# Kernel optimization log

Hardware: AMD Instinct MI355X
Metric: run time of the kernel (lower is better)

## Reference

```python
import jax, jax.numpy as jnp
import numpy as np

NUM_HEADS = 2
DIM_NODE = 100
DIM_EDGE = 100
DIM_TIME = 100
DIM_OUT = 100
N_DST = 32768
N_EDGE = 524288
LN_EPS = 1e-5


def setup_inputs() -> dict:
    key = jax.random.key(0)
    ks = jax.random.split(key, 12)
    dst_h = jax.random.normal(ks[0], (N_DST, DIM_NODE), dtype=jnp.float32)
    src_h = jax.random.normal(ks[1], (N_EDGE, DIM_NODE), dtype=jnp.float32)
    efeat = jax.random.normal(ks[2], (N_EDGE, DIM_EDGE), dtype=jnp.float32)
    # time deltas are non-negative elapsed times
    time_deltas = jax.random.uniform(ks[3], (N_EDGE,), dtype=jnp.float32) * 1000.0
    edge_dst = jnp.sort(jax.random.randint(ks[4], (N_EDGE,), 0, N_DST, dtype=jnp.int32))
    # TimeEncode: fixed geometric frequencies, zero bias
    time_w = jnp.asarray(1.0 / 10 ** np.linspace(0, 9, DIM_TIME), dtype=jnp.float32)
    time_b = jnp.zeros((DIM_TIME,), dtype=jnp.float32)
    def lin(k, fan_out, fan_in):
        s = 1.0 / np.sqrt(fan_in)
        return jax.random.uniform(k, (fan_out, fan_in), jnp.float32, -s, s)
    wq_w = lin(ks[5], DIM_OUT, DIM_NODE + DIM_TIME)
    wq_b = jax.random.normal(ks[6], (DIM_OUT,), jnp.float32) * 0.02
    wkv_w = lin(ks[7], 2 * DIM_OUT, DIM_NODE + DIM_EDGE + DIM_TIME)
    wkv_b = jax.random.normal(ks[8], (2 * DIM_OUT,), jnp.float32) * 0.02
    wout_w = lin(ks[9], DIM_OUT, DIM_NODE + DIM_OUT)
    wout_b = jax.random.normal(ks[10], (DIM_OUT,), jnp.float32) * 0.02
    ln_g = jnp.ones((DIM_OUT,), jnp.float32)
    ln_b = jnp.zeros((DIM_OUT,), jnp.float32)
    return dict(dst_h=dst_h, src_h=src_h, efeat=efeat, time_deltas=time_deltas,
                edge_dst=edge_dst, time_w=time_w, time_b=time_b,
                wq_w=wq_w, wq_b=wq_b, wkv_w=wkv_w, wkv_b=wkv_b,
                wout_w=wout_w, wout_b=wout_b, ln_g=ln_g, ln_b=ln_b)


def reference(dst_h, src_h, efeat, time_deltas, edge_dst, time_w, time_b,
              wq_w, wq_b, wkv_w, wkv_b, wout_w, wout_b, ln_g, ln_b):
    n_dst = dst_h.shape[0]
    dim_out = wq_w.shape[0]
    dh = dim_out // NUM_HEADS
    # TimeEncode: cos(w*t + b); zero-time feature for dst nodes
    zero_tf = jnp.broadcast_to(jnp.cos(time_b), (n_dst, time_b.shape[0]))
    nbr_tf = jnp.cos(time_deltas[:, None] * time_w[None, :] + time_b)  # [E, dim_time]
    Q = jnp.concatenate([dst_h, zero_tf], axis=1) @ wq_w.T + wq_b       # [N_dst, dim_out]
    Z = jnp.concatenate([src_h, efeat, nbr_tf], axis=1) @ wkv_w.T + wkv_b  # [E, 2*dim_out]
    K = Z[:, :dim_out].reshape(-1, NUM_HEADS, dh)
    V = Z[:, dim_out:].reshape(-1, NUM_HEADS, dh)
    Qe = Q[edge_dst].reshape(-1, NUM_HEADS, dh)  # edge_view gather
    attn = jnp.sum(Qe * K, axis=2)               # [E, H]
    attn = jax.nn.leaky_relu(attn, negative_slope=0.2)
    # edge_softmax: segment softmax over edges grouped by dst
    m = jax.ops.segment_max(attn, edge_dst, num_segments=n_dst)
    e = jnp.exp(attn - m[edge_dst])
    s = jax.ops.segment_sum(e, edge_dst, num_segments=n_dst)
    a = e / s[edge_dst]                           # [E, H]
    out_e = (V * a[:, :, None]).reshape(-1, dim_out)
    out = jax.ops.segment_sum(out_e, edge_dst, num_segments=n_dst)  # edge_reduce sum
    out = jnp.concatenate([out, dst_h], axis=1) @ wout_w.T + wout_b
    out = jax.nn.relu(out)  # dropout disabled (eval)
    mu = jnp.mean(out, axis=-1, keepdims=True)
    var = jnp.var(out, axis=-1, keepdims=True)
    return (out - mu) / jnp.sqrt(var + LN_EPS) * ln_g + ln_b
```

## Files before the change

### kernel.cpp

```cpp
#include <hip/hip_runtime.h>
#include <math.h>

#define N_DST   32768
#define N_EDGE  524288
#define LN_EPS  1e-5f

typedef __attribute__((ext_vector_type(8))) short short8b;
typedef __attribute__((ext_vector_type(4))) float f32x4;

static __device__ __forceinline__ unsigned short f2bf(float f) {
    unsigned u = __float_as_uint(f);
    u += 0x7fff + ((u >> 16) & 1);
    return (unsigned short)(u >> 16);
}
static __device__ __forceinline__ float bf2f(unsigned short s) {
    return __uint_as_float(((unsigned)s) << 16);
}

__global__ void k_prep(const float* __restrict__ wkv_w, const float* __restrict__ wq_w,
                       const float* __restrict__ wq_b, const float* __restrict__ time_b,
                       const float* __restrict__ wout_w,
                       float* __restrict__ zq, float* __restrict__ wout_t,
                       unsigned short* __restrict__ Bv) {
    int idx = blockIdx.x * 256 + threadIdx.x;
    if (idx < 100) {
        float acc = wq_b[idx];
        for (int j = 0; j < 100; ++j)
            acc += cosf(time_b[j]) * wq_w[idx * 200 + 100 + j];
        zq[idx] = acc;
    } else if (idx < 20100) {
        int r = idx - 100;
        wout_t[r] = wout_w[(size_t)(r % 100) * 200 + r / 100];
    } else if (idx < 95364) {
        int r2 = idx - 20100;
        int jj = r2 & 7, l = (r2 >> 3) & 63, nf = (r2 >> 9) % 7, kc = r2 / 3584;
        int j = kc * 32 + ((l >> 4) << 3) + jj;
        int o = nf * 16 + (l & 15);
        float v = (j < 600 && o < 100 && (j / 300 == o / 50))
                  ? wkv_w[(size_t)(100 + o) * 300 + (j % 300)] : 0.f;
        Bv[r2] = f2bf(v);
    }
}

__global__ void k_precomp(const float* __restrict__ wq_w, const float* __restrict__ wkv_w,
                          const float* __restrict__ wkv_b, const float* __restrict__ zq,
                          unsigned short* __restrict__ Bq, float* __restrict__ C2) {
    int idx = blockIdx.x * 256 + threadIdx.x;
    if (idx < 77824) {
        int jj = idx & 7, l = (idx >> 3) & 63, nf = (idx >> 9) % 19, kcp = idx / 9728;
        int kc = kcp & 3, p = kcp >> 2;
        int i = kc * 32 + ((l >> 4) << 3) + jj;
        int j = p * 304 + nf * 16 + (l & 15);
        float acc = 0.f;
        if (i < 100 && j < 602) {
            if (j < 600) {
                int h = j / 300, cc = j % 300;
                const float* __restrict__ wq = wq_w + (size_t)(h * 50) * 200 + i;
                const float* __restrict__ wk = wkv_w + (size_t)(h * 50) * 300 + cc;
                #pragma unroll 10
                for (int d = 0; d < 50; ++d)
                    acc = fmaf(wq[(size_t)d * 200], wk[(size_t)d * 300], acc);
            } else {
                int h = j - 600;
                const float* __restrict__ wq = wq_w + (size_t)(h * 50) * 200 + i;
                for (int d = 0; d < 50; ++d)
                    acc = fmaf(wq[(size_t)d * 200], wkv_b[h * 50 + d], acc);
            }
        }
        Bq[idx] = f2bf(acc);
    } else if (idx < 78426) {
        int j = idx - 77824;
        float acc = 0.f;
        if (j < 600) {
            int h = j / 300, cc = j % 300;
            for (int d = 0; d < 50; ++d)
                acc = fmaf(zq[h * 50 + d], wkv_w[(size_t)(h * 50 + d) * 300 + cc], acc);
        } else {
            int h = j - 600;
            for (int d = 0; d < 50; ++d)
                acc = fmaf(zq[h * 50 + d], wkv_b[h * 50 + d], acc);
        }
        C2[j] = acc;
    }
}

__global__ void k_offsets(const int* __restrict__ dst, int* __restrict__ off) {
    int n = blockIdx.x * 256 + threadIdx.x;
    if (n > N_DST) return;
    int lo = 0, hi = N_EDGE;
    while (lo < hi) {
        int mid = (lo + hi) >> 1;
        if (dst[mid] < n) lo = mid + 1; else hi = mid;
    }
    off[n] = lo;
}

__global__ __launch_bounds__(256, 1) void k_qw(
        const float* __restrict__ dst_h, const unsigned short* __restrict__ Bq,
        const float* __restrict__ C2, unsigned short* __restrict__ QW) {
    __shared__ alignas(16) unsigned short Bs[9728];
    const int t = threadIdx.x, lane = t & 63;
    const int g = blockIdx.x * 4 + (t >> 6);
    const int col = lane & 15, slice = lane >> 4;
    const int row = g * 16 + col;

    short8b af[4];
    {
        const float* __restrict__ dr = dst_h + (size_t)row * 100;
        #pragma unroll
        for (int kc = 0; kc < 4; ++kc) {
            int k0 = kc * 32 + slice * 8;
            float4 xa = make_float4(0.f, 0.f, 0.f, 0.f), xb = xa;
            if (k0 + 8 <= 100) { xa = *(const float4*)(dr + k0); xb = *(const float4*)(dr + k0 + 4); }
            else if (k0 < 100)  { xa = *(const float4*)(dr + k0); }
            short8b a;
            a[0] = (short)f2bf(xa.x); a[1] = (short)f2bf(xa.y);
            a[2] = (short)f2bf(xa.z); a[3] = (short)f2bf(xa.w);
            a[4] = (short)f2bf(xb.x); a[5] = (short)f2bf(xb.y);
            a[6] = (short)f2bf(xb.z); a[7] = (short)f2bf(xb.w);
            af[kc] = a;
        }
    }
    const int re0 = g * 16 + (slice << 2);
    #pragma unroll
    for (int p = 0; p < 2; ++p) {
        f32x4 acc[19];
        #pragma unroll
        for (int nf = 0; nf < 19; ++nf) {
            int c = p * 304 + nf * 16 + col;
            float b = (c < 602) ? C2[c] : 0.f;
            acc[nf] = (f32x4){b, b, b, b};
        }
        #pragma unroll
        for (int kc = 0; kc < 4; ++kc) {
            {
                const float4* __restrict__ ws4 = (const float4*)Bq + (size_t)(p * 4 + kc) * 1216;
                float4* __restrict__ wd = (float4*)Bs;
                #pragma unroll
                for (int i = 0; i < 4; ++i) wd[i * 256 + t] = ws4[i * 256 + t];
                if (t < 192) wd[1024 + t] = ws4[1024 + t];
            }
            __syncthreads();
            #pragma unroll
            for (int nf = 0; nf < 19; ++nf) {
                short8b w = *(const short8b*)(&Bs[(size_t)(nf * 64 + lane) * 8]);
                acc[nf] = __builtin_amdgcn_mfma_f32_16x16x32_bf16(af[kc], w, acc[nf], 0, 0, 0);
            }
            __syncthreads();
        }
        #pragma unroll
        for (int nf = 0; nf < 19; ++nf) {
            int c = p * 304 + nf * 16 + col;
            if (c < 602) {
                #pragma unroll
                for (int r = 0; r < 4; ++r)
                    QW[(size_t)(re0 + r) * 608 + c] = f2bf(acc[nf][r]);
            }
        }
    }
}

__global__ __launch_bounds__(256) void k_node(
        const float* __restrict__ src_h, const float* __restrict__ efeat,
        const float* __restrict__ td,
        const float* __restrict__ time_w, const float* __restrict__ time_b,
        const unsigned short* __restrict__ QW, const int* __restrict__ off,
        unsigned short* __restrict__ Xagg) {
    const int lane = threadIdx.x & 63;
    const int n = blockIdx.x * 4 + (threadIdx.x >> 6);
    const int r0 = off[n], cnt = off[n + 1] - r0;
    unsigned short* __restrict__ xo = Xagg + (size_t)n * 600;
    if (cnt <= 0) {
        #pragma unroll
        for (int s = 0; s < 5; ++s) {
            int cc = s * 64 + lane;
            if (cc < 300) { xo[cc] = 0; xo[300 + cc] = 0; }
        }
        return;
    }
    float qw0[5], qw1[5];
    #pragma unroll
    for (int s = 0; s < 5; ++s) {
        int cc = s * 64 + lane;
        qw0[s] = (cc < 300) ? bf2f(QW[(size_t)n * 608 + cc])       : 0.f;
        qw1[s] = (cc < 300) ? bf2f(QW[(size_t)n * 608 + 300 + cc]) : 0.f;
    }
    const float B0 = bf2f(QW[(size_t)n * 608 + 600]);
    const float B1 = bf2f(QW[(size_t)n * 608 + 601]);
    float tw3 = 0.f, tb3 = 0.f, tw4 = 0.f, tb4 = 0.f;
    if (lane >= 8) { tw3 = time_w[lane - 8]; tb3 = time_b[lane - 8]; }
    if (lane < 44) { tw4 = time_w[56 + lane]; tb4 = time_b[56 + lane]; }

    auto LOADX = [&](float* x, int r) {
        const float* __restrict__ sr = src_h + (size_t)r * 100;
        const float* __restrict__ er = efeat + (size_t)r * 100;
        const float tdv = td[r];
        x[0] = sr[lane];
        x[1] = (lane < 36) ? sr[64 + lane] : er[lane - 36];
        x[2] = er[28 + lane];
        x[3] = (lane < 8) ? er[92 + lane] : __cosf(fmaf(tdv, tw3, tb3));
        x[4] = (lane < 44) ? __cosf(fmaf(tdv, tw4, tb4)) : 0.f;
    };

    float m0 = -1e30f, m1 = -1e30f, sum0 = 0.f, sum1 = 0.f;
    float a0[5] = {0.f, 0.f, 0.f, 0.f, 0.f}, a1[5] = {0.f, 0.f, 0.f, 0.f, 0.f};

    auto UPDATE = [&](float l0, float l1, const float* x) {
        l0 = l0 > 0.f ? l0 : 0.2f * l0;
        l1 = l1 > 0.f ? l1 : 0.2f * l1;
        if (l0 <= m0 && l1 <= m1) {
            float w0 = __expf(l0 - m0), w1 = __expf(l1 - m1);
            sum0 += w0; sum1 += w1;
            #pragma unroll
            for (int s = 0; s < 5; ++s) {
                a0[s] = fmaf(w0, x[s], a0[s]);
                a1[s] = fmaf(w1, x[s], a1[s]);
            }
        } else {
            float m0n = fmaxf(m0, l0), m1n = fmaxf(m1, l1);
            float r0f = __expf(m0 - m0n), r1f = __expf(m1 - m1n);
            float w0 = __expf(l0 - m0n),  w1 = __expf(l1 - m1n);
            sum0 = fmaf(sum0, r0f, w0);
            sum1 = fmaf(sum1, r1f, w1);
            #pragma unroll
            for (int s = 0; s < 5; ++s) {
                a0[s] = fmaf(a0[s], r0f, w0 * x[s]);
                a1[s] = fmaf(a1[s], r1f, w1 * x[s]);
            }
            m0 = m0n; m1 = m1n;
        }
    };

    float xA[5], xB[5], xC[5], xD[5];
    int i = 0;
    if (cnt >= 2) {
        LOADX(xA, r0); LOADX(xB, r0 + 1);
        for (; i + 2 <= cnt; i += 2) {
            float pA0 = 0.f, pA1 = 0.f, pB0 = 0.f, pB1 = 0.f;
            #pragma unroll
            for (int s = 0; s < 5; ++s) {
                pA0 = fmaf(xA[s], qw0[s], pA0); pA1 = fmaf(xA[s], qw1[s], pA1);
                pB0 = fmaf(xB[s], qw0[s], pB0); pB1 = fmaf(xB[s], qw1[s], pB1);
            }
            #pragma unroll
            for (int sh = 1; sh < 64; sh <<= 1) {
                pA0 += __shfl_xor(pA0, sh); pA1 += __shfl_xor(pA1, sh);
                pB0 += __shfl_xor(pB0, sh); pB1 += __shfl_xor(pB1, sh);
            }
            if (i + 2 < cnt) LOADX(xC, r0 + i + 2);
            if (i + 3 < cnt) LOADX(xD, r0 + i + 3);
            UPDATE(pA0 + B0, pA1 + B1, xA);
            UPDATE(pB0 + B0, pB1 + B1, xB);
            #pragma unroll
            for (int s = 0; s < 5; ++s) { xA[s] = xC[s]; xB[s] = xD[s]; }
        }
    } else {
        LOADX(xA, r0);
    }
    if (i < cnt) {
        float p0 = 0.f, p1 = 0.f;
        #pragma unroll
        for (int s = 0; s < 5; ++s) {
            p0 = fmaf(xA[s], qw0[s], p0);
            p1 = fmaf(xA[s], qw1[s], p1);
        }
        #pragma unroll
        for (int sh = 1; sh < 64; sh <<= 1) {
            p0 += __shfl_xor(p0, sh); p1 += __shfl_xor(p1, sh);
        }
        UPDATE(p0 + B0, p1 + B1, xA);
    }
    const float inv0 = 1.f / sum0, inv1 = 1.f / sum1;
    #pragma unroll
    for (int s = 0; s < 5; ++s) {
        int cc = s * 64 + lane;
        if (cc < 300) {
            xo[cc]       = f2bf(a0[s] * inv0);
            xo[300 + cc] = f2bf(a1[s] * inv1);
        }
    }
}

__global__ __launch_bounds__(256, 1) void k_aggv(
        const unsigned short* __restrict__ Xagg, const unsigned short* __restrict__ Bv,
        const float* __restrict__ wkv_b, const int* __restrict__ off,
        float* __restrict__ agg) {
    __shared__ alignas(16) unsigned short Bs[10752];
    const int t = threadIdx.x, lane = t & 63;
    const int g = blockIdx.x * 4 + (t >> 6);
    const int col = lane & 15, slice = lane >> 4;
    const int row = g * 16 + col;

    short8b af[21];
    {
        const unsigned short* __restrict__ xr = Xagg + (size_t)row * 600;
        #pragma unroll
        for (int kc = 0; kc < 21; ++kc) {
            int j0 = kc * 32 + slice * 8;
            if (j0 + 8 <= 600) {
                af[kc] = *(const short8b*)(xr + j0);
            } else {
                short8b z; 
                #pragma unroll
                for (int q = 0; q < 8; ++q) z[q] = 0;
                af[kc] = z;
            }
        }
    }
    f32x4 acc[7];
    #pragma unroll
    for (int nf = 0; nf < 7; ++nf) acc[nf] = (f32x4){0.f, 0.f, 0.f, 0.f};

    #pragma unroll
    for (int slab = 0; slab < 7; ++slab) {
        {
            const float4* __restrict__ ws4 = (const float4*)Bv + (size_t)slab * 1344;
            float4* __restrict__ wd = (float4*)Bs;
            #pragma unroll
            for (int i = 0; i < 5; ++i) wd[i * 256 + t] = ws4[i * 256 + t];
            if (t < 64) wd[1280 + t] = ws4[1280 + t];
        }
        __syncthreads();
        #pragma unroll
        for (int kl = 0; kl < 3; ++kl) {
            const int kc = slab * 3 + kl;
            #pragma unroll
            for (int nf = 0; nf < 7; ++nf) {
                short8b w = *(const short8b*)(&Bs[(size_t)((kl * 7 + nf) * 64 + lane) * 8]);
                acc[nf] = __builtin_amdgcn_mfma_f32_16x16x32_bf16(af[kc], w, acc[nf], 0, 0, 0);
            }
        }
        __syncthreads();
    }
    const int re0 = g * 16 + (slice << 2);
    #pragma unroll
    for (int nf = 0; nf < 7; ++nf) {
        int o = nf * 16 + col;
        if (o < 100) {
            float bv = wkv_b[100 + o];
            #pragma unroll
            for (int r = 0; r < 4; ++r) {
                int node = re0 + r;
                bool has = off[node + 1] > off[node];
                agg[(size_t)node * 100 + o] = acc[nf][r] + (has ? bv : 0.f);
            }
        }
    }
}

__global__ __launch_bounds__(128) void k_out(const float* __restrict__ agg,
                                             const float* __restrict__ dst_h,
                                             const float* __restrict__ wout_t,
                                             const float* __restrict__ wout_b,
                                             const float* __restrict__ ln_g,
                                             const float* __restrict__ ln_b,
                                             float* __restrict__ out) {
    __shared__ float Fs[8][200];
    __shared__ float red[8][128];
    const int n0 = blockIdx.x * 8, t = threadIdx.x;
    for (int idx = t; idx < 1600; idx += 128) {
        int n = idx / 200, i = idx % 200;
        Fs[n][i] = (i < 100) ? agg[(size_t)(n0 + n) * 100 + i]
                             : dst_h[(size_t)(n0 + n) * 100 + (i - 100)];
    }
    __syncthreads();
    float v[8] = {0.f, 0.f, 0.f, 0.f, 0.f, 0.f, 0.f, 0.f};
    if (t < 100) {
        float b = wout_b[t];
        #pragma unroll
        for (int n = 0; n < 8; ++n) v[n] = b;
        for (int i = 0; i < 200; ++i) {
            float w = wout_t[i * 100 + t];
            #pragma unroll
            for (int n = 0; n < 8; ++n) v[n] = fmaf(Fs[n][i], w, v[n]);
        }
        #pragma unroll
        for (int n = 0; n < 8; ++n) v[n] = fmaxf(v[n], 0.f);
    }
    #pragma unroll
    for (int n = 0; n < 8; ++n) red[n][t] = (t < 100) ? v[n] : 0.f;
    __syncthreads();
    for (int s = 64; s > 0; s >>= 1) {
        if (t < s) {
            #pragma unroll
            for (int n = 0; n < 8; ++n) red[n][t] += red[n][t + s];
        }
        __syncthreads();
    }
    float mu[8];
    #pragma unroll
    for (int n = 0; n < 8; ++n) mu[n] = red[n][0] * 0.01f;
    __syncthreads();
    #pragma unroll
    for (int n = 0; n < 8; ++n) {
        float dv = (t < 100) ? (v[n] - mu[n]) : 0.f;
        red[n][t] = dv * dv;
    }
    __syncthreads();
    for (int s = 64; s > 0; s >>= 1) {
        if (t < s) {
            #pragma unroll
            for (int n = 0; n < 8; ++n) red[n][t] += red[n][t + s];
        }
        __syncthreads();
    }
    if (t < 100) {
        #pragma unroll
        for (int n = 0; n < 8; ++n) {
            float var = red[n][0] * 0.01f;
            out[(size_t)(n0 + n) * 100 + t] =
                (v[n] - mu[n]) * rsqrtf(var + LN_EPS) * ln_g[t] + ln_b[t];
        }
    }
}

extern "C" void kernel_launch(void* const* d_in, const int* in_sizes, int n_in,
                              void* d_out, int out_size, void* d_ws, size_t ws_size,
                              hipStream_t stream) {
    const float* dst_h   = (const float*)d_in[0];
    const float* src_h   = (const float*)d_in[1];
    const float* efeat   = (const float*)d_in[2];
    const float* td      = (const float*)d_in[3];
    const int*   edst    = (const int*)  d_in[4];
    const float* time_w  = (const float*)d_in[5];
    const float* time_b  = (const float*)d_in[6];
    const float* wq_w    = (const float*)d_in[7];
    const float* wq_b    = (const float*)d_in[8];
    const float* wkv_w   = (const float*)d_in[9];
    const float* wkv_b   = (const float*)d_in[10];
    const float* wout_w  = (const float*)d_in[11];
    const float* wout_b  = (const float*)d_in[12];
    const float* ln_g    = (const float*)d_in[13];
    const float* ln_b    = (const float*)d_in[14];
    float* out = (float*)d_out;

    char* ws = (char*)d_ws;
    size_t off = 0;
    auto carve = [&](size_t bytes) { char* p = ws + off; off = (off + bytes + 255) & ~(size_t)255; return p; };
    unsigned short* QW    = (unsigned short*)carve((size_t)N_DST * 608 * 2);
    unsigned short* Xagg  = (unsigned short*)carve((size_t)N_DST * 600 * 2);
    float*          agg   = (float*)carve((size_t)N_DST * 100 * 4);
    float*          C2    = (float*)carve(602 * 4);
    unsigned short* Bq    = (unsigned short*)carve(77824 * 2);
    unsigned short* Bv    = (unsigned short*)carve(75264 * 2);
    float*          woutT = (float*)carve(20000 * 4);
    float*          zq    = (float*)carve(100 * 4);
    int*            offs  = (int*)carve((size_t)(N_DST + 1) * 4);

    k_prep<<<(95364 + 255) / 256, 256, 0, stream>>>(wkv_w, wq_w, wq_b, time_b, wout_w,
                                                    zq, woutT, Bv);
    k_precomp<<<(78426 + 255) / 256, 256, 0, stream>>>(wq_w, wkv_w, wkv_b, zq, Bq, C2);
    k_offsets<<<(N_DST + 1 + 255) / 256, 256, 0, stream>>>(edst, offs);
    k_qw<<<N_DST / 64, 256, 0, stream>>>(dst_h, Bq, C2, QW);
    k_node<<<N_DST / 4, 256, 0, stream>>>(src_h, efeat, td, time_w, time_b,
                                          QW, offs, Xagg);
    k_aggv<<<N_DST / 64, 256, 0, stream>>>(Xagg, Bv, wkv_b, offs, agg);
    k_out<<<N_DST / 8, 128, 0, stream>>>(agg, dst_h, woutT, wout_b, ln_g, ln_b, out);
}
```

Measured before the change: 314.1 us.

## Process four edges per wavefront concurrently in k_node with 16-lane groups

Restructures the per-node aggregation kernel so each 64-lane wavefront splits into four 16-lane groups, each handling a different edge at the same time. Each lane now holds 19 feature slots instead of 5. The score reduction shrinks from a 64-lane to a 16-lane shuffle, and the online-softmax max is shared across the groups. The aim is to shorten the serial per-edge dependency chain and raise memory-level parallelism. In exchange it needs more registers and a final cross-group shuffle reduction of the accumulators, and lanes sit idle when a node's edge count is not a multiple of four.

```diff
diff --git a/kernel.cpp b/kernel.cpp
--- a/kernel.cpp
+++ b/kernel.cpp
@@ -167,116 +167,122 @@
         const unsigned short* __restrict__ QW, const int* __restrict__ off,
         unsigned short* __restrict__ Xagg) {
     const int lane = threadIdx.x & 63;
+    const int grp = lane >> 4, li = lane & 15;
     const int n = blockIdx.x * 4 + (threadIdx.x >> 6);
     const int r0 = off[n], cnt = off[n + 1] - r0;
     unsigned short* __restrict__ xo = Xagg + (size_t)n * 600;
     if (cnt <= 0) {
         #pragma unroll
-        for (int s = 0; s < 5; ++s) {
-            int cc = s * 64 + lane;
-            if (cc < 300) { xo[cc] = 0; xo[300 + cc] = 0; }
+        for (int s = 0; s < 19; ++s) {
+            if ((s & 3) == grp) {
+                int cc = s * 16 + li;
+                if (cc < 300) { xo[cc] = 0; xo[300 + cc] = 0; }
+            }
         }
         return;
     }
-    float qw0[5], qw1[5];
-    #pragma unroll
-    for (int s = 0; s < 5; ++s) {
-        int cc = s * 64 + lane;
+    float qw0[19], qw1[19];
+    #pragma unroll
+    for (int s = 0; s < 19; ++s) {
+        int cc = s * 16 + li;
         qw0[s] = (cc < 300) ? bf2f(QW[(size_t)n * 608 + cc])       : 0.f;
         qw1[s] = (cc < 300) ? bf2f(QW[(size_t)n * 608 + 300 + cc]) : 0.f;
     }
     const float B0 = bf2f(QW[(size_t)n * 608 + 600]);
     const float B1 = bf2f(QW[(size_t)n * 608 + 601]);
-    float tw3 = 0.f, tb3 = 0.f, tw4 = 0.f, tb4 = 0.f;
-    if (lane >= 8) { tw3 = time_w[lane - 8]; tb3 = time_b[lane - 8]; }
-    if (lane < 44) { tw4 = time_w[56 + lane]; tb4 = time_b[56 + lane]; }
-
-    auto LOADX = [&](float* x, int r) {
-        const float* __restrict__ sr = src_h + (size_t)r * 100;
-        const float* __restrict__ er = efeat + (size_t)r * 100;
-        const float tdv = td[r];
-        x[0] = sr[lane];
-        x[1] = (lane < 36) ? sr[64 + lane] : er[lane - 36];
-        x[2] = er[28 + lane];
-        x[3] = (lane < 8) ? er[92 + lane] : __cosf(fmaf(tdv, tw3, tb3));
-        x[4] = (lane < 44) ? __cosf(fmaf(tdv, tw4, tb4)) : 0.f;
-    };
+    float tWc[7], tBc[7];
+    #pragma unroll
+    for (int q = 0; q < 7; ++q) {
+        int j = (12 + q) * 16 + li - 200;
+        bool v = (j >= 0 && j < 100);
+        tWc[q] = v ? time_w[j] : 0.f;
+        tBc[q] = v ? time_b[j] : 0.f;
+    }
 
     float m0 = -1e30f, m1 = -1e30f, sum0 = 0.f, sum1 = 0.f;
-    float a0[5] = {0.f, 0.f, 0.f, 0.f, 0.f}, a1[5] = {0.f, 0.f, 0.f, 0.f, 0.f};
-
-    auto UPDATE = [&](float l0, float l1, const float* x) {
+    float a0[19], a1[19];
+    #pragma unroll
+    for (int s = 0; s < 19; ++s) { a0[s] = 0.f; a1[s] = 0.f; }
+
+    for (int i = 0; i < cnt; i += 4) {
+        const int e = i + grp;
+        const bool valid = (e < cnt);
+        const int r = r0 + (valid ? e : 0);
+        float x[19];
+        {
+            const float* __restrict__ sr = src_h + (size_t)r * 100;
+            const float* __restrict__ er = efeat + (size_t)r * 100;
+            const float tdv = valid ? td[r] : 0.f;
+            #pragma unroll
+            for (int s = 0; s < 19; ++s) {
+                int cc = s * 16 + li;
+                float v;
+                if (s < 6)        v = sr[cc];
+                else if (s == 6)  v = (li < 4) ? sr[96 + li] : er[li - 4];
+                else if (s < 12)  v = er[cc - 100];
+                else if (s == 12) v = (li < 8) ? er[92 + li]
+                                               : __cosf(fmaf(tdv, tWc[0], tBc[0]));
+                else if (s < 18)  v = __cosf(fmaf(tdv, tWc[s - 12], tBc[s - 12]));
+                else              v = (li < 12) ? __cosf(fmaf(tdv, tWc[6], tBc[6])) : 0.f;
+                x[s] = valid ? v : 0.f;
+            }
+        }
+        float p0 = 0.f, p1 = 0.f;
+        #pragma unroll
+        for (int s = 0; s < 19; ++s) {
+            p0 = fmaf(x[s], qw0[s], p0);
+            p1 = fmaf(x[s], qw1[s], p1);
+        }
+        #pragma unroll
+        for (int sh = 1; sh < 16; sh <<= 1) {
+            p0 += __shfl_xor(p0, sh);
+            p1 += __shfl_xor(p1, sh);
+        }
+        float l0 = p0 + B0, l1 = p1 + B1;
         l0 = l0 > 0.f ? l0 : 0.2f * l0;
         l1 = l1 > 0.f ? l1 : 0.2f * l1;
-        if (l0 <= m0 && l1 <= m1) {
+        if (!valid) { l0 = -1e30f; l1 = -1e30f; }
+        float mx0 = l0, mx1 = l1;
+        mx0 = fmaxf(mx0, __shfl_xor(mx0, 16)); mx1 = fmaxf(mx1, __shfl_xor(mx1, 16));
+        mx0 = fmaxf(mx0, __shfl_xor(mx0, 32)); mx1 = fmaxf(mx1, __shfl_xor(mx1, 32));
+        if (mx0 <= m0 && mx1 <= m1) {
             float w0 = __expf(l0 - m0), w1 = __expf(l1 - m1);
             sum0 += w0; sum1 += w1;
             #pragma unroll
-            for (int s = 0; s < 5; ++s) {
+            for (int s = 0; s < 19; ++s) {
                 a0[s] = fmaf(w0, x[s], a0[s]);
                 a1[s] = fmaf(w1, x[s], a1[s]);
             }
         } else {
-            float m0n = fmaxf(m0, l0), m1n = fmaxf(m1, l1);
+            float m0n = fmaxf(m0, mx0), m1n = fmaxf(m1, mx1);
             float r0f = __expf(m0 - m0n), r1f = __expf(m1 - m1n);
             float w0 = __expf(l0 - m0n),  w1 = __expf(l1 - m1n);
             sum0 = fmaf(sum0, r0f, w0);
             sum1 = fmaf(sum1, r1f, w1);
             #pragma unroll
-            for (int s = 0; s < 5; ++s) {
+            for (int s = 0; s < 19; ++s) {
                 a0[s] = fmaf(a0[s], r0f, w0 * x[s]);
                 a1[s] = fmaf(a1[s], r1f, w1 * x[s]);
             }
             m0 = m0n; m1 = m1n;
         }
-    };
-
-    float xA[5], xB[5], xC[5], xD[5];
-    int i = 0;
-    if (cnt >= 2) {
-        LOADX(xA, r0); LOADX(xB, r0 + 1);
-        for (; i + 2 <= cnt; i += 2) {
-            float pA0 = 0.f, pA1 = 0.f, pB0 = 0.f, pB1 = 0.f;
-            #pragma unroll
-            for (int s = 0; s < 5; ++s) {
-                pA0 = fmaf(xA[s], qw0[s], pA0); pA1 = fmaf(xA[s], qw1[s], pA1);
-                pB0 = fmaf(xB[s], qw0[s], pB0); pB1 = fmaf(xB[s], qw1[s], pB1);
-            }
-            #pragma unroll
-            for (int sh = 1; sh < 64; sh <<= 1) {
-                pA0 += __shfl_xor(pA0, sh); pA1 += __shfl_xor(pA1, sh);
-                pB0 += __shfl_xor(pB0, sh); pB1 += __shfl_xor(pB1, sh);
-            }
-            if (i + 2 < cnt) LOADX(xC, r0 + i + 2);
-            if (i + 3 < cnt) LOADX(xD, r0 + i + 3);
-            UPDATE(pA0 + B0, pA1 + B1, xA);
-            UPDATE(pB0 + B0, pB1 + B1, xB);
-            #pragma unroll
-            for (int s = 0; s < 5; ++s) { xA[s] = xC[s]; xB[s] = xD[s]; }
-        }
-    } else {
-        LOADX(xA, r0);
-    }
-    if (i < cnt) {
-        float p0 = 0.f, p1 = 0.f;
-        #pragma unroll
-        for (int s = 0; s < 5; ++s) {
-            p0 = fmaf(xA[s], qw0[s], p0);
-            p1 = fmaf(xA[s], qw1[s], p1);
-        }
-        #pragma unroll
-        for (int sh = 1; sh < 64; sh <<= 1) {
-            p0 += __shfl_xor(p0, sh); p1 += __shfl_xor(p1, sh);
-        }
-        UPDATE(p0 + B0, p1 + B1, xA);
-    }
+    }
+    #pragma unroll
+    for (int s = 0; s < 19; ++s) {
+        a0[s] += __shfl_xor(a0[s], 16); a0[s] += __shfl_xor(a0[s], 32);
+        a1[s] += __shfl_xor(a1[s], 16); a1[s] += __shfl_xor(a1[s], 32);
+    }
+    sum0 += __shfl_xor(sum0, 16); sum0 += __shfl_xor(sum0, 32);
+    sum1 += __shfl_xor(sum1, 16); sum1 += __shfl_xor(sum1, 32);
     const float inv0 = 1.f / sum0, inv1 = 1.f / sum1;
     #pragma unroll
-    for (int s = 0; s < 5; ++s) {
-        int cc = s * 64 + lane;
-        if (cc < 300) {
-            xo[cc]       = f2bf(a0[s] * inv0);
-            xo[300 + cc] = f2bf(a1[s] * inv1);
+    for (int s = 0; s < 19; ++s) {
+        if ((s & 3) == grp) {
+            int cc = s * 16 + li;
+            if (cc < 300) {
+                xo[cc]       = f2bf(a0[s] * inv0);
+                xo[300 + cc] = f2bf(a1[s] * inv1);
+            }
         }
     }
 }
@@ -300,7 +306,7 @@
             if (j0 + 8 <= 600) {
                 af[kc] = *(const short8b*)(xr + j0);
             } else {
-                short8b z; 
+                short8b z;
                 #pragma unroll
                 for (int q = 0; q < 8; ++q) z[q] = 0;
                 af[kc] = z;
```

New measurement: 301.0 us, median of 2. -4.2%, faster.
